# Kernel optimization log

Hardware: AMD Instinct MI355X
Metric: run time of the kernel (lower is better)

## Reference

```python
import jax, jax.numpy as jnp
import numpy as np

B, L, D = 4, 512, 512
VOCAB = 32000
SEMB_NUM = 4
SEG = VOCAB // SEMB_NUM
TEMP = float(np.power(512, 0.5))  # sqrt(d_model)
NEG_INF = 1e9  # hparams.inf
INIT_RANGE = 0.1


def setup_inputs() -> dict:
    key = jax.random.key(0)
    k1, k2, k3 = jax.random.split(key, 3)
    q = jax.random.normal(k1, (B, L, D), dtype=jnp.float32)
    x_rank = jax.random.randint(k2, (B, L), 0, SEMB_NUM)
    emb = jax.random.uniform(k3, (VOCAB, D), dtype=jnp.float32,
                             minval=-INIT_RANGE, maxval=INIT_RANGE)
    return {"q": q, "x_rank": x_rank, "emb": emb}


def reference(q, x_rank, emb):
    # segment id of each vocab entry: [V]
    seg_id = jnp.arange(VOCAB) // SEG
    # mask == True means "blocked": token with x_rank==i only sees segment i
    mask = seg_id[None, None, :] != x_rank[:, :, None]          # [B, L, V]
    scores = jnp.einsum('bld,vd->blv', q, emb) / TEMP           # [B, L, V]
    scores = jnp.where(mask, -NEG_INF, scores)
    attn = jax.nn.softmax(scores, axis=-1)
    attn = jnp.where(mask, 0.0, attn)  # masked_fill_ after softmax (dropout=0, eval)
    ctx = jnp.einsum('blv,vd->bld', attn, emb)                  # [B, L, D]
    return ctx + q  # residual add (no char_gate)
```

## Files before the change

kernel.cpp:

```cpp
#include <hip/hip_runtime.h>
#include <math.h>


constexpr int Dm   = 512;
constexpr int SEG  = 8000;
constexpr int PSTR = 8064;
constexpr int NTOK = 2048;
constexpr int TIL  = 128;
constexpr int MAXTILES = 20;
constexpr int MAXSLOTS = MAXTILES * TIL;

constexpr size_t WS_DENOM = 0;
constexpr size_t WS_META  = 8192;
constexpr size_t WS_PERM  = 8448;
constexpr size_t WS_QB8   = 32768;
constexpr size_t WS_EB8   = WS_QB8 + (size_t)MAXSLOTS * Dm;
constexpr size_t WS_OACC  = WS_EB8 + (size_t)32000 * Dm;
constexpr size_t WS_ET8   = WS_OACC + (size_t)8 * Dm * MAXSLOTS * 2;
constexpr size_t WS_P8    = WS_ET8 + (size_t)Dm * 32000;

typedef __attribute__((ext_vector_type(4))) float f32x4;
typedef __attribute__((ext_vector_type(4))) unsigned int u32x4;
#define LDSP __attribute__((address_space(3)))
typedef LDSP unsigned char lds_u8;
typedef LDSP u32x4 lds_v4;

static __device__ __forceinline__ ushort f2bf(float f) {
    union { float f; unsigned u; } v; v.f = f;
    unsigned r = v.u + 0x7FFF + ((v.u >> 16) & 1);
    return (ushort)(r >> 16);
}
static __device__ __forceinline__ float bf2f(ushort u) {
    union { unsigned u; float f; } v; v.u = ((unsigned)u) << 16;
    return v.f;
}
static __device__ __forceinline__ int pack_fp8x4(float a, float b, float c, float d) {
    int r = __builtin_amdgcn_cvt_pk_fp8_f32(a, b, 0, false);
    r = __builtin_amdgcn_cvt_pk_fp8_f32(c, d, r, true);
    return r;
}

#define WAIT0 asm volatile("s_waitcnt vmcnt(0)" ::: "memory")
#define LGKM0 asm volatile("s_waitcnt lgkmcnt(0)" ::: "memory")
#define BARX  { __builtin_amdgcn_s_barrier(); __builtin_amdgcn_sched_barrier(0); }

#define CSTEP(CUR)                                                             \
    {                                                                          \
        long A[4], B[4];                                                       \
        const int cg0 = (quad >> 1), ho = (quad & 1) * 8;                      \
        _Pragma("unroll")                                                      \
        for (int m = 0; m < 4; ++m) {                                          \
            const int row = rh*64 + m*16 + l15;                                \
            A[m] = *(const LDSP long*)((CUR) + row*128 + ((cg0) ^ (row & 7))*16 + ho);\
        }                                                                      \
        _Pragma("unroll")                                                      \
        for (int n = 0; n < 4; ++n) {                                          \
            const int row = th*64 + n*16 + l15;                                \
            B[n] = *(const LDSP long*)((CUR) + row*128 + ((4 + cg0) ^ (row & 7))*16 + ho);\
        }                                                                      \
        __builtin_amdgcn_s_setprio(1);                                         \
        _Pragma("unroll")                                                      \
        for (int m = 0; m < 4; ++m)                                            \
            _Pragma("unroll")                                                  \
            for (int n = 0; n < 4; ++n)                                        \
                acc[m][n] = __builtin_amdgcn_mfma_f32_16x16x32_fp8_fp8(A[m], B[n], acc[m][n], 0, 0, 0); \
        __builtin_amdgcn_s_setprio(0);                                         \
        _Pragma("unroll")                                                      \
        for (int m = 0; m < 4; ++m) {                                          \
            const int row = rh*64 + m*16 + l15;                                \
            A[m] = *(const LDSP long*)((CUR) + row*128 + ((2 + cg0) ^ (row & 7))*16 + ho);\
        }                                                                      \
        _Pragma("unroll")                                                      \
        for (int n = 0; n < 4; ++n) {                                          \
            const int row = th*64 + n*16 + l15;                                \
            B[n] = *(const LDSP long*)((CUR) + row*128 + ((6 + cg0) ^ (row & 7))*16 + ho);\
        }                                                                      \
        __builtin_amdgcn_s_setprio(1);                                         \
        _Pragma("unroll")                                                      \
        for (int m = 0; m < 4; ++m)                                            \
            _Pragma("unroll")                                                  \
            for (int n = 0; n < 4; ++n)                                        \
                acc[m][n] = __builtin_amdgcn_mfma_f32_16x16x32_fp8_fp8(A[m], B[n], acc[m][n], 0, 0, 0); \
        __builtin_amdgcn_s_setprio(0);                                         \
    }

#define PSTEP(CUR, NXT, TIN)                                                   \
    {                                                                          \
        u32x4 st0 = *(const u32x4*)(pre[0] + (TIN)*64);                        \
        u32x4 st1 = *(const u32x4*)(pre[1] + (TIN)*64);                        \
        u32x4 st2 = *(const u32x4*)(pre[2] + (TIN)*64);                        \
        u32x4 st3 = *(const u32x4*)(pre[3] + (TIN)*64);                        \
        CSTEP(CUR)                                                             \
        WAIT0;                                                                 \
        *(lds_v4*)((NXT) + (w*256 +   0 + lane)*16) = st0;                     \
        *(lds_v4*)((NXT) + (w*256 +  64 + lane)*16) = st1;                     \
        *(lds_v4*)((NXT) + (w*256 + 128 + lane)*16) = st2;                     \
        *(lds_v4*)((NXT) + (w*256 + 192 + lane)*16) = st3;                     \
        LGKM0; BARX;                                                           \
    }

#define PROLOG(DST, TI0)                                                       \
    {                                                                          \
        u32x4 st0 = *(const u32x4*)(pre[0] + (TI0)*64);                        \
        u32x4 st1 = *(const u32x4*)(pre[1] + (TI0)*64);                        \
        u32x4 st2 = *(const u32x4*)(pre[2] + (TI0)*64);                        \
        u32x4 st3 = *(const u32x4*)(pre[3] + (TI0)*64);                        \
        WAIT0;                                                                 \
        *(lds_v4*)((DST) + (w*256 +   0 + lane)*16) = st0;                     \
        *(lds_v4*)((DST) + (w*256 +  64 + lane)*16) = st1;                     \
        *(lds_v4*)((DST) + (w*256 + 128 + lane)*16) = st2;                     \
        *(lds_v4*)((DST) + (w*256 + 192 + lane)*16) = st3;                     \
        LGKM0; BARX;                                                           \
    }

__global__ __launch_bounds__(256)
void k_conv(const float* __restrict__ emb, unsigned char* __restrict__ EB8,
            unsigned char* __restrict__ ET8,
            const int* __restrict__ xr, int* __restrict__ meta,
            int* __restrict__ perm, float* __restrict__ denom) {
    __shared__ unsigned char sT[64 * 8 * 16];
    const int tid = threadIdx.x;
    if (blockIdx.x == 250) {
        if (blockIdx.y != 0) return;
        __shared__ int cnt[4], base[5], cur[4];
        if (tid < 4) { cnt[tid] = 0; cur[tid] = 0; }
        __syncthreads();
        for (int t = tid; t < NTOK; t += 256) {
            atomicAdd(&cnt[xr[t]], 1);
            denom[t] = 0.f;
        }
        __syncthreads();
        if (tid == 0) {
            base[0] = 0;
            for (int r = 0; r < 4; ++r) base[r+1] = base[r] + ((cnt[r] + TIL - 1) / TIL) * TIL;
            for (int r = 0; r < 5; ++r) meta[r] = base[r];
        }
        __syncthreads();
        for (int s = tid; s < MAXSLOTS; s += 256) perm[s] = -1;
        __syncthreads();
        for (int t = tid; t < NTOK; t += 256) {
            int r = xr[t];
            perm[base[r] + atomicAdd(&cur[r], 1)] = t;
        }
        return;
    }
    const int r0 = blockIdx.x * 128, d0 = blockIdx.y * 64;
    {
        const int dq = tid & 15, ro = tid >> 4;
        int p[8];
        #pragma unroll
        for (int i = 0; i < 8; ++i) {
            float4 v = *(const float4*)(emb + (size_t)(r0 + ro*8 + i) * Dm + d0 + dq*4);
            p[i] = pack_fp8x4(v.x, v.y, v.z, v.w);
            *(int*)(EB8 + (size_t)(r0 + ro*8 + i) * Dm + d0 + dq*4) = p[i];
        }
        const int gr = ro >> 1, half = ro & 1;
        #pragma unroll
        for (int j = 0; j < 4; ++j) {
            const int d = dq*4 + j;
            unsigned long long t = 0;
            #pragma unroll
            for (int i = 0; i < 8; ++i)
                t |= ((unsigned long long)((p[i] >> (8*j)) & 0xff)) << (8*i);
            *(unsigned long long*)(sT + (d*8 + (gr ^ (d & 7))) * 16 + half * 8) = t;
        }
    }
    __syncthreads();
    {
        const int d = tid >> 2, rq = tid & 3;
        unsigned char* dst = ET8 + (size_t)(d0 + d) * 32000 + r0;
        #pragma unroll
        for (int b = 0; b < 2; ++b) {
            const int gr = rq * 2 + b;
            *(uint4*)(dst + gr * 16) = *(const uint4*)(sT + (d*8 + (gr ^ (d & 7))) * 16);
        }
    }
}

__global__ __launch_bounds__(256)
void k_qb(const float* __restrict__ q, const int* __restrict__ perm,
          unsigned char* __restrict__ Qb8) {
    const int slot = blockIdx.x * 8 + (threadIdx.x >> 5);
    const int ln = threadIdx.x & 31;
    const int tok = perm[slot];
    #pragma unroll
    for (int j = 0; j < 4; ++j) {
        const int c4 = ln + j * 32;
        int p = 0;
        if (tok >= 0) {
            float4 v = ((const float4*)q)[(size_t)tok * 128 + c4];
            p = pack_fp8x4(v.x, v.y, v.z, v.w);
        }
        ((int*)(Qb8 + (size_t)slot * Dm))[c4] = p;
    }
}

__global__ __launch_bounds__(256, 4)
void k_qk(const unsigned char* __restrict__ EB8, const unsigned char* __restrict__ Qb8,
          const int* __restrict__ meta, const int* __restrict__ perm,
          float* __restrict__ denom, unsigned char* __restrict__ P8) {
    __shared__ unsigned char s0[128 * 128];
    __shared__ unsigned char s1[128 * 128];
    const int tid = threadIdx.x, lane = tid & 63, w = tid >> 6;
    const int g    = blockIdx.x & 7;
    const int rest = blockIdx.x >> 3;
    const int tt       = rest >> 3;
    const int rt_local = rest & 7;
    const int c = g * 8 + rt_local;
    const int slot0 = tt * TIL;
    const int b1 = meta[1], b2 = meta[2], b3 = meta[3], b4 = meta[4];
    if (slot0 >= b4) return;
    const int row0 = c * 128;
    if (row0 >= PSTR) return;
    const int rank = (slot0 >= b1) + (slot0 >= b2) + (slot0 >= b3);

    const unsigned char* pre[4];
    #pragma unroll
    for (int i = 0; i < 4; ++i) {
        const int gg = w * 256 + i * 64 + lane;
        const int r = gg >> 3, u = gg & 7, cg = u ^ (r & 7);
        if (cg < 4) {
            int grow = row0 + r;
            if (grow >= SEG) grow = SEG - 1;
            pre[i] = EB8 + (size_t)rank * SEG * Dm + (size_t)grow * Dm + cg * 16;
        } else {
            pre[i] = Qb8 + (size_t)(slot0 + r) * Dm + (cg - 4) * 16;
        }
    }
    const int rh = w >> 1, th = w & 1, quad = lane >> 4, l15 = lane & 15;
    const float invT = 0.04419417382415922f;
    lds_u8* b0p = (lds_u8*)s0;
    lds_u8* b1p = (lds_u8*)s1;

    f32x4 acc[4][4] = {};
    PROLOG(b0p, 0)
    PSTEP(b0p, b1p, 1)
    PSTEP(b1p, b0p, 2)
    PSTEP(b0p, b1p, 3)
    PSTEP(b1p, b0p, 4)
    PSTEP(b0p, b1p, 5)
    PSTEP(b1p, b0p, 6)
    PSTEP(b0p, b1p, 7)
    CSTEP(b1p)

    float dsum[4] = {0.f, 0.f, 0.f, 0.f};
    #pragma unroll
    for (int m = 0; m < 4; ++m) {
        const int r4 = row0 + rh*64 + m*16 + quad*4;
        if (r4 < SEG) {
            #pragma unroll
            for (int n = 0; n < 4; ++n) {
                float e0 = __expf(acc[m][n][0] * invT);
                float e1 = __expf(acc[m][n][1] * invT);
                float e2 = __expf(acc[m][n][2] * invT);
                float e3 = __expf(acc[m][n][3] * invT);
                const int slot = slot0 + th*64 + n*16 + l15;
                *(int*)(P8 + (size_t)slot * PSTR + r4) = pack_fp8x4(e0, e1, e2, e3);
                dsum[n] += e0 + e1 + e2 + e3;
            }
        } else if (r4 < PSTR) {
            #pragma unroll
            for (int n = 0; n < 4; ++n) {
                const int slot = slot0 + th*64 + n*16 + l15;
                *(int*)(P8 + (size_t)slot * PSTR + r4) = 0;
            }
        }
    }
    #pragma unroll
    for (int n = 0; n < 4; ++n) {
        float s = dsum[n];
        s += __shfl_xor(s, 16, 64);
        s += __shfl_xor(s, 32, 64);
        if (quad == 0) {
            const int tok = perm[slot0 + th*64 + n*16 + l15];
            if (tok >= 0) atomicAdd(denom + tok, s);
        }
    }
}

__global__ __launch_bounds__(256, 4)
void k_pv(const unsigned char* __restrict__ ET8, const unsigned char* __restrict__ P8,
          const int* __restrict__ meta, ushort* __restrict__ Oacc) {
    __shared__ unsigned char s0[128 * 128];
    __shared__ unsigned char s1[128 * 128];
    const int tid = threadIdx.x, lane = tid & 63, w = tid >> 6;
    const int z    = blockIdx.x & 7;
    const int rest = blockIdx.x >> 3;
    const int tt   = rest >> 2;
    const int dt   = rest & 3;
    const int slot0 = tt * TIL;
    const int b1 = meta[1], b2 = meta[2], b3 = meta[3], b4 = meta[4];
    if (slot0 >= b4) return;
    const int rank = (slot0 >= b1) + (slot0 >= b2) + (slot0 >= b3);
    const int d0 = dt * 128;
    const int kstart = z * 1024;
    const int nit = (z == 7) ? 14 : 16;

    const unsigned char* pre[4];
    #pragma unroll
    for (int i = 0; i < 4; ++i) {
        const int gg = w * 256 + i * 64 + lane;
        const int r = gg >> 3, u = gg & 7, cg = u ^ (r & 7);
        if (cg < 4)
            pre[i] = ET8 + (size_t)(d0 + r) * 32000 + (size_t)rank * SEG + kstart + cg * 16;
        else
            pre[i] = P8 + (size_t)(slot0 + r) * PSTR + kstart + (cg - 4) * 16;
    }
    const int rh = w >> 1, th = w & 1, quad = lane >> 4, l15 = lane & 15;
    lds_u8* b0p = (lds_u8*)s0;
    lds_u8* b1p = (lds_u8*)s1;

    f32x4 acc[4][4] = {};
    PROLOG(b0p, 0)
    for (int t2 = 0; t2 < nit/2 - 1; ++t2) {
        PSTEP(b0p, b1p, 2*t2 + 1)
        PSTEP(b1p, b0p, 2*t2 + 2)
    }
    PSTEP(b0p, b1p, nit - 1)
    CSTEP(b1p)

    ushort* Oz = Oacc + (size_t)z * Dm * MAXSLOTS;
    #pragma unroll
    for (int m = 0; m < 4; ++m) {
        const int d4 = d0 + rh*64 + m*16 + quad*4;
        #pragma unroll
        for (int n = 0; n < 4; ++n) {
            const int slot = slot0 + th*64 + n*16 + l15;
            #pragma unroll
            for (int j = 0; j < 4; ++j)
                Oz[(size_t)(d4 + j) * MAXSLOTS + slot] = f2bf(acc[m][n][j]);
        }
    }
}

__global__ __launch_bounds__(256)
void k_final(const float* __restrict__ q, const int* __restrict__ meta,
             const int* __restrict__ perm, const float* __restrict__ denom,
             const ushort* __restrict__ Oacc, float* __restrict__ out) {
    const int d = blockIdx.x;
    const int ns = meta[4];
    for (int s = threadIdx.x; s < ns; s += 256) {
        const int tok = perm[s];
        if (tok < 0) continue;
        float v = 0.f;
        #pragma unroll
        for (int z = 0; z < 8; ++z)
            v += bf2f(Oacc[((size_t)z * Dm + d) * MAXSLOTS + s]);
        out[(size_t)tok * Dm + d] = v / denom[tok] + q[(size_t)tok * Dm + d];
    }
}

extern "C" void kernel_launch(void* const* d_in, const int* in_sizes, int n_in,
                              void* d_out, int out_size, void* d_ws, size_t ws_size,
                              hipStream_t stream) {
    const float* q   = (const float*)d_in[0];
    const int*   xr  = (const int*)d_in[1];
    const float* emb = (const float*)d_in[2];
    float* out = (float*)d_out;
    char* ws = (char*)d_ws;

    float*  denom        = (float*)(ws + WS_DENOM);
    int*    meta         = (int*)(ws + WS_META);
    int*    perm         = (int*)(ws + WS_PERM);
    unsigned char* Qb8   = (unsigned char*)(ws + WS_QB8);
    unsigned char* EB8   = (unsigned char*)(ws + WS_EB8);
    ushort* Oacc         = (ushort*)(ws + WS_OACC);
    unsigned char* ET8   = (unsigned char*)(ws + WS_ET8);
    unsigned char* P8    = (unsigned char*)(ws + WS_P8);

    k_conv<<<dim3(251, 8), 256, 0, stream>>>(emb, EB8, ET8, xr, meta, perm, denom);
    k_qb<<<MAXSLOTS / 8, 256, 0, stream>>>(q, perm, Qb8);
    k_qk<<<8 * 8 * MAXTILES, 256, 0, stream>>>(EB8, Qb8, meta, perm, denom, P8);
    k_pv<<<8 * 4 * MAXTILES, 256, 0, stream>>>(ET8, P8, meta, Oacc);
    k_final<<<Dm, 256, 0, stream>>>(q, meta, perm, denom, Oacc, out);
}
```

Measured before the change: 191.0 us.

## Double K-step per stage in QK/PV GEMMs and token-major final reduction

The QK and PV fp8 GEMM kernels now stage a full 128-byte K slice of both operands per pipeline step, in separate LDS buffers, instead of 64 bytes of each packed into one buffer. This halves the number of barrier-synchronised steps while doubling LDS use, so launch bounds drop from 4 to 2 blocks per CU. The final kernel is reorganised to iterate per token using a new inverse permutation written in k_conv, so that output and q rows are accessed contiguously with float4 stores. The cost is lower occupancy and strided Oacc reads in the final kernel.

```diff
diff --git a/kernel.cpp b/kernel.cpp
--- a/kernel.cpp
+++ b/kernel.cpp
@@ -13,6 +13,7 @@
 constexpr size_t WS_DENOM = 0;
 constexpr size_t WS_META  = 8192;
 constexpr size_t WS_PERM  = 8448;
+constexpr size_t WS_IPERM = 20480;
 constexpr size_t WS_QB8   = 32768;
 constexpr size_t WS_EB8   = WS_QB8 + (size_t)MAXSLOTS * Dm;
 constexpr size_t WS_OACC  = WS_EB8 + (size_t)32000 * Dm;
@@ -44,19 +45,20 @@
 #define LGKM0 asm volatile("s_waitcnt lgkmcnt(0)" ::: "memory")
 #define BARX  { __builtin_amdgcn_s_barrier(); __builtin_amdgcn_sched_barrier(0); }
 
-#define CSTEP(CUR)                                                             \
-    {                                                                          \
+#define CSTEP(CA, CB)                                                          \
+    _Pragma("unroll")                                                          \
+    for (int ks = 0; ks < 4; ++ks) {                                           \
+        const int cg = ks*2 + (quad >> 1), ho = (quad & 1) * 8;                \
         long A[4], B[4];                                                       \
-        const int cg0 = (quad >> 1), ho = (quad & 1) * 8;                      \
         _Pragma("unroll")                                                      \
         for (int m = 0; m < 4; ++m) {                                          \
             const int row = rh*64 + m*16 + l15;                                \
-            A[m] = *(const LDSP long*)((CUR) + row*128 + ((cg0) ^ (row & 7))*16 + ho);\
+            A[m] = *(const LDSP long*)((CA) + (row*8 + (cg ^ (row & 7)))*16 + ho); \
         }                                                                      \
         _Pragma("unroll")                                                      \
         for (int n = 0; n < 4; ++n) {                                          \
             const int row = th*64 + n*16 + l15;                                \
-            B[n] = *(const LDSP long*)((CUR) + row*128 + ((4 + cg0) ^ (row & 7))*16 + ho);\
+            B[n] = *(const LDSP long*)((CB) + (row*8 + (cg ^ (row & 7)))*16 + ho); \
         }                                                                      \
         __builtin_amdgcn_s_setprio(1);                                         \
         _Pragma("unroll")                                                      \
@@ -65,51 +67,40 @@
             for (int n = 0; n < 4; ++n)                                        \
                 acc[m][n] = __builtin_amdgcn_mfma_f32_16x16x32_fp8_fp8(A[m], B[n], acc[m][n], 0, 0, 0); \
         __builtin_amdgcn_s_setprio(0);                                         \
-        _Pragma("unroll")                                                      \
-        for (int m = 0; m < 4; ++m) {                                          \
-            const int row = rh*64 + m*16 + l15;                                \
-            A[m] = *(const LDSP long*)((CUR) + row*128 + ((2 + cg0) ^ (row & 7))*16 + ho);\
-        }                                                                      \
-        _Pragma("unroll")                                                      \
-        for (int n = 0; n < 4; ++n) {                                          \
-            const int row = th*64 + n*16 + l15;                                \
-            B[n] = *(const LDSP long*)((CUR) + row*128 + ((6 + cg0) ^ (row & 7))*16 + ho);\
-        }                                                                      \
-        __builtin_amdgcn_s_setprio(1);                                         \
-        _Pragma("unroll")                                                      \
-        for (int m = 0; m < 4; ++m)                                            \
-            _Pragma("unroll")                                                  \
-            for (int n = 0; n < 4; ++n)                                        \
-                acc[m][n] = __builtin_amdgcn_mfma_f32_16x16x32_fp8_fp8(A[m], B[n], acc[m][n], 0, 0, 0); \
-        __builtin_amdgcn_s_setprio(0);                                         \
-    }
-
-#define PSTEP(CUR, NXT, TIN)                                                   \
+    }
+
+#define PSTEP(CA, CB, NA, NB, T)                                               \
     {                                                                          \
-        u32x4 st0 = *(const u32x4*)(pre[0] + (TIN)*64);                        \
-        u32x4 st1 = *(const u32x4*)(pre[1] + (TIN)*64);                        \
-        u32x4 st2 = *(const u32x4*)(pre[2] + (TIN)*64);                        \
-        u32x4 st3 = *(const u32x4*)(pre[3] + (TIN)*64);                        \
-        CSTEP(CUR)                                                             \
+        u32x4 sv[8];                                                           \
+        _Pragma("unroll")                                                      \
+        for (int i = 0; i < 4; ++i) {                                          \
+            sv[i]   = *(const u32x4*)(srcA[i] + (size_t)(T)*128);              \
+            sv[4+i] = *(const u32x4*)(srcB[i] + (size_t)(T)*128);              \
+        }                                                                      \
+        CSTEP(CA, CB)                                                          \
         WAIT0;                                                                 \
-        *(lds_v4*)((NXT) + (w*256 +   0 + lane)*16) = st0;                     \
-        *(lds_v4*)((NXT) + (w*256 +  64 + lane)*16) = st1;                     \
-        *(lds_v4*)((NXT) + (w*256 + 128 + lane)*16) = st2;                     \
-        *(lds_v4*)((NXT) + (w*256 + 192 + lane)*16) = st3;                     \
+        _Pragma("unroll")                                                      \
+        for (int i = 0; i < 4; ++i) {                                          \
+            *(lds_v4*)((NA) + dst[i]) = sv[i];                                 \
+            *(lds_v4*)((NB) + dst[i]) = sv[4+i];                               \
+        }                                                                      \
         LGKM0; BARX;                                                           \
     }
 
-#define PROLOG(DST, TI0)                                                       \
+#define PROLOG(DA, DB)                                                         \
     {                                                                          \
-        u32x4 st0 = *(const u32x4*)(pre[0] + (TI0)*64);                        \
-        u32x4 st1 = *(const u32x4*)(pre[1] + (TI0)*64);                        \
-        u32x4 st2 = *(const u32x4*)(pre[2] + (TI0)*64);                        \
-        u32x4 st3 = *(const u32x4*)(pre[3] + (TI0)*64);                        \
+        u32x4 sv[8];                                                           \
+        _Pragma("unroll")                                                      \
+        for (int i = 0; i < 4; ++i) {                                          \
+            sv[i]   = *(const u32x4*)(srcA[i]);                                \
+            sv[4+i] = *(const u32x4*)(srcB[i]);                                \
+        }                                                                      \
         WAIT0;                                                                 \
-        *(lds_v4*)((DST) + (w*256 +   0 + lane)*16) = st0;                     \
-        *(lds_v4*)((DST) + (w*256 +  64 + lane)*16) = st1;                     \
-        *(lds_v4*)((DST) + (w*256 + 128 + lane)*16) = st2;                     \
-        *(lds_v4*)((DST) + (w*256 + 192 + lane)*16) = st3;                     \
+        _Pragma("unroll")                                                      \
+        for (int i = 0; i < 4; ++i) {                                          \
+            *(lds_v4*)((DA) + dst[i]) = sv[i];                                 \
+            *(lds_v4*)((DB) + dst[i]) = sv[4+i];                               \
+        }                                                                      \
         LGKM0; BARX;                                                           \
     }
 
@@ -117,7 +108,8 @@
 void k_conv(const float* __restrict__ emb, unsigned char* __restrict__ EB8,
             unsigned char* __restrict__ ET8,
             const int* __restrict__ xr, int* __restrict__ meta,
-            int* __restrict__ perm, float* __restrict__ denom) {
+            int* __restrict__ perm, int* __restrict__ iperm,
+            float* __restrict__ denom) {
     __shared__ unsigned char sT[64 * 8 * 16];
     const int tid = threadIdx.x;
     if (blockIdx.x == 250) {
@@ -140,7 +132,9 @@
         __syncthreads();
         for (int t = tid; t < NTOK; t += 256) {
             int r = xr[t];
-            perm[base[r] + atomicAdd(&cur[r], 1)] = t;
+            int sl = base[r] + atomicAdd(&cur[r], 1);
+            perm[sl] = t;
+            iperm[t] = sl;
         }
         return;
     }
@@ -195,12 +189,14 @@
     }
 }
 
-__global__ __launch_bounds__(256, 4)
+__global__ __launch_bounds__(256, 2)
 void k_qk(const unsigned char* __restrict__ EB8, const unsigned char* __restrict__ Qb8,
           const int* __restrict__ meta, const int* __restrict__ perm,
           float* __restrict__ denom, unsigned char* __restrict__ P8) {
-    __shared__ unsigned char s0[128 * 128];
-    __shared__ unsigned char s1[128 * 128];
+    __shared__ unsigned char sA0[128 * 128];
+    __shared__ unsigned char sB0[128 * 128];
+    __shared__ unsigned char sA1[128 * 128];
+    __shared__ unsigned char sB1[128 * 128];
     const int tid = threadIdx.x, lane = tid & 63, w = tid >> 6;
     const int g    = blockIdx.x & 7;
     const int rest = blockIdx.x >> 3;
@@ -214,34 +210,30 @@
     if (row0 >= PSTR) return;
     const int rank = (slot0 >= b1) + (slot0 >= b2) + (slot0 >= b3);
 
-    const unsigned char* pre[4];
+    const unsigned char* srcA[4];
+    const unsigned char* srcB[4];
+    int dst[4];
     #pragma unroll
     for (int i = 0; i < 4; ++i) {
         const int gg = w * 256 + i * 64 + lane;
-        const int r = gg >> 3, u = gg & 7, cg = u ^ (r & 7);
-        if (cg < 4) {
-            int grow = row0 + r;
-            if (grow >= SEG) grow = SEG - 1;
-            pre[i] = EB8 + (size_t)rank * SEG * Dm + (size_t)grow * Dm + cg * 16;
-        } else {
-            pre[i] = Qb8 + (size_t)(slot0 + r) * Dm + (cg - 4) * 16;
-        }
+        const int r = gg >> 3, cg = gg & 7;
+        int grow = row0 + r;
+        if (grow >= SEG) grow = SEG - 1;
+        srcA[i] = EB8 + (size_t)rank * SEG * Dm + (size_t)grow * Dm + cg * 16;
+        srcB[i] = Qb8 + (size_t)(slot0 + r) * Dm + cg * 16;
+        dst[i]  = (r * 8 + (cg ^ (r & 7))) * 16;
     }
     const int rh = w >> 1, th = w & 1, quad = lane >> 4, l15 = lane & 15;
     const float invT = 0.04419417382415922f;
-    lds_u8* b0p = (lds_u8*)s0;
-    lds_u8* b1p = (lds_u8*)s1;
+    lds_u8* a0 = (lds_u8*)sA0; lds_u8* b0 = (lds_u8*)sB0;
+    lds_u8* a1 = (lds_u8*)sA1; lds_u8* b1p = (lds_u8*)sB1;
 
     f32x4 acc[4][4] = {};
-    PROLOG(b0p, 0)
-    PSTEP(b0p, b1p, 1)
-    PSTEP(b1p, b0p, 2)
-    PSTEP(b0p, b1p, 3)
-    PSTEP(b1p, b0p, 4)
-    PSTEP(b0p, b1p, 5)
-    PSTEP(b1p, b0p, 6)
-    PSTEP(b0p, b1p, 7)
-    CSTEP(b1p)
+    PROLOG(a0, b0)
+    PSTEP(a0, b0, a1, b1p, 1)
+    PSTEP(a1, b1p, a0, b0, 2)
+    PSTEP(a0, b0, a1, b1p, 3)
+    CSTEP(a1, b1p)
 
     float dsum[4] = {0.f, 0.f, 0.f, 0.f};
     #pragma unroll
@@ -278,11 +270,13 @@
     }
 }
 
-__global__ __launch_bounds__(256, 4)
+__global__ __launch_bounds__(256, 2)
 void k_pv(const unsigned char* __restrict__ ET8, const unsigned char* __restrict__ P8,
           const int* __restrict__ meta, ushort* __restrict__ Oacc) {
-    __shared__ unsigned char s0[128 * 128];
-    __shared__ unsigned char s1[128 * 128];
+    __shared__ unsigned char sA0[128 * 128];
+    __shared__ unsigned char sB0[128 * 128];
+    __shared__ unsigned char sA1[128 * 128];
+    __shared__ unsigned char sB1[128 * 128];
     const int tid = threadIdx.x, lane = tid & 63, w = tid >> 6;
     const int z    = blockIdx.x & 7;
     const int rest = blockIdx.x >> 3;
@@ -294,30 +288,32 @@
     const int rank = (slot0 >= b1) + (slot0 >= b2) + (slot0 >= b3);
     const int d0 = dt * 128;
     const int kstart = z * 1024;
-    const int nit = (z == 7) ? 14 : 16;
-
-    const unsigned char* pre[4];
+    const int nit = (z == 7) ? 7 : 8;
+
+    const unsigned char* srcA[4];
+    const unsigned char* srcB[4];
+    int dst[4];
     #pragma unroll
     for (int i = 0; i < 4; ++i) {
         const int gg = w * 256 + i * 64 + lane;
-        const int r = gg >> 3, u = gg & 7, cg = u ^ (r & 7);
-        if (cg < 4)
-            pre[i] = ET8 + (size_t)(d0 + r) * 32000 + (size_t)rank * SEG + kstart + cg * 16;
-        else
-            pre[i] = P8 + (size_t)(slot0 + r) * PSTR + kstart + (cg - 4) * 16;
+        const int r = gg >> 3, cg = gg & 7;
+        srcA[i] = ET8 + (size_t)(d0 + r) * 32000 + (size_t)rank * SEG + kstart + cg * 16;
+        srcB[i] = P8 + (size_t)(slot0 + r) * PSTR + kstart + cg * 16;
+        dst[i]  = (r * 8 + (cg ^ (r & 7))) * 16;
     }
     const int rh = w >> 1, th = w & 1, quad = lane >> 4, l15 = lane & 15;
-    lds_u8* b0p = (lds_u8*)s0;
-    lds_u8* b1p = (lds_u8*)s1;
+    lds_u8* cA = (lds_u8*)sA0; lds_u8* cB = (lds_u8*)sB0;
+    lds_u8* nA = (lds_u8*)sA1; lds_u8* nB = (lds_u8*)sB1;
 
     f32x4 acc[4][4] = {};
-    PROLOG(b0p, 0)
-    for (int t2 = 0; t2 < nit/2 - 1; ++t2) {
-        PSTEP(b0p, b1p, 2*t2 + 1)
-        PSTEP(b1p, b0p, 2*t2 + 2)
-    }
-    PSTEP(b0p, b1p, nit - 1)
-    CSTEP(b1p)
+    PROLOG(cA, cB)
+    for (int t = 1; t < nit; ++t) {
+        PSTEP(cA, cB, nA, nB, t)
+        lds_u8* tp;
+        tp = cA; cA = nA; nA = tp;
+        tp = cB; cB = nB; nB = tp;
+    }
+    CSTEP(cA, cB)
 
     ushort* Oz = Oacc + (size_t)z * Dm * MAXSLOTS;
     #pragma unroll
@@ -334,19 +330,30 @@
 }
 
 __global__ __launch_bounds__(256)
-void k_final(const float* __restrict__ q, const int* __restrict__ meta,
-             const int* __restrict__ perm, const float* __restrict__ denom,
-             const ushort* __restrict__ Oacc, float* __restrict__ out) {
-    const int d = blockIdx.x;
-    const int ns = meta[4];
-    for (int s = threadIdx.x; s < ns; s += 256) {
-        const int tok = perm[s];
-        if (tok < 0) continue;
-        float v = 0.f;
-        #pragma unroll
-        for (int z = 0; z < 8; ++z)
-            v += bf2f(Oacc[((size_t)z * Dm + d) * MAXSLOTS + s]);
-        out[(size_t)tok * Dm + d] = v / denom[tok] + q[(size_t)tok * Dm + d];
+void k_final(const float* __restrict__ q, const int* __restrict__ iperm,
+             const float* __restrict__ denom, const ushort* __restrict__ Oacc,
+             float* __restrict__ out) {
+    const int tk = threadIdx.x >> 5;
+    const int dl = threadIdx.x & 31;
+    const int token = blockIdx.x * 8 + tk;
+    const int s = iperm[token];
+    const float inv = 1.0f / denom[token];
+    const float* qrow = q + (size_t)token * Dm;
+    float* orow = out + (size_t)token * Dm;
+    #pragma unroll
+    for (int dc = 0; dc < 4; ++dc) {
+        const int d = dc * 128 + dl * 4;
+        float v[4];
+        #pragma unroll
+        for (int j = 0; j < 4; ++j) {
+            float a = 0.f;
+            #pragma unroll
+            for (int z = 0; z < 8; ++z)
+                a += bf2f(Oacc[((size_t)z * Dm + d + j) * MAXSLOTS + s]);
+            v[j] = a * inv + qrow[d + j];
+        }
+        float4 o; o.x = v[0]; o.y = v[1]; o.z = v[2]; o.w = v[3];
+        *(float4*)(orow + d) = o;
     }
 }
 
@@ -362,15 +369,16 @@
     float*  denom        = (float*)(ws + WS_DENOM);
     int*    meta         = (int*)(ws + WS_META);
     int*    perm         = (int*)(ws + WS_PERM);
+    int*    iperm        = (int*)(ws + WS_IPERM);
     unsigned char* Qb8   = (unsigned char*)(ws + WS_QB8);
     unsigned char* EB8   = (unsigned char*)(ws + WS_EB8);
     ushort* Oacc         = (ushort*)(ws + WS_OACC);
     unsigned char* ET8   = (unsigned char*)(ws + WS_ET8);
     unsigned char* P8    = (unsigned char*)(ws + WS_P8);
 
-    k_conv<<<dim3(251, 8), 256, 0, stream>>>(emb, EB8, ET8, xr, meta, perm, denom);
+    k_conv<<<dim3(251, 8), 256, 0, stream>>>(emb, EB8, ET8, xr, meta, perm, iperm, denom);
     k_qb<<<MAXSLOTS / 8, 256, 0, stream>>>(q, perm, Qb8);
     k_qk<<<8 * 8 * MAXTILES, 256, 0, stream>>>(EB8, Qb8, meta, perm, denom, P8);
     k_pv<<<8 * 4 * MAXTILES, 256, 0, stream>>>(ET8, P8, meta, Oacc);
-    k_final<<<Dm, 256, 0, stream>>>(q, meta, perm, denom, Oacc, out);
-}
+    k_final<<<NTOK / 8, 256, 0, stream>>>(q, iperm, denom, Oacc, out);
+}
```

Result: slower. 210.6 us (+10.3%).
